# Kernel tuning notes

Hardware: AMD Instinct MI355X
Metric: run time of the kernel (lower is better)

Reference implementation:

```python
import jax, jax.numpy as jnp
import numpy as np
import math

D = 768; H = 12; DH = 64; LAT = 512; B = 2; L = 1024


def _rms(x, w, eps=1e-6):
    return w * x * jax.lax.rsqrt(jnp.mean(x * x, axis=-1, keepdims=True) + eps)


def _rope_tables(seq_len, dh):
    inv = 1.0 / (10000.0 ** (np.arange(0, dh, 2, dtype=np.float32) / dh))
    t = np.arange(seq_len, dtype=np.float32)
    f = np.outer(t, inv)
    emb = np.concatenate([f, f], axis=-1)
    return jnp.asarray(np.cos(emb))[None, :, None, :], jnp.asarray(np.sin(emb))[None, :, None, :]


def _rope(x, cos, sin):
    x1, x2 = jnp.split(x, 2, axis=-1)
    return x * cos + jnp.concatenate([-x2, x1], axis=-1) * sin


def setup_inputs():
    key = jax.random.key(0)
    ks = jax.random.split(key, 8)
    s = 0.02
    return {
        'x': jax.random.normal(ks[0], (B, L, D), jnp.float32),
        'w_ln': jnp.ones((D,), jnp.float32),
        'w_compress': jax.random.normal(ks[1], (D, LAT), jnp.float32) * s,
        'w_qkv': jax.random.normal(ks[2], (LAT, 3 * D), jnp.float32) * s,
        'w_reso': jax.random.normal(ks[3], (LAT, H * 4), jnp.float32) * s,
        'w_qn': jnp.ones((DH,), jnp.float32),
        'w_kn': jnp.ones((DH,), jnp.float32),
        'head_decay': jnp.linspace(-3.0, 1.0, H).astype(jnp.float32),
        'temperature': jnp.ones((1,), jnp.float32) * 0.5,
        'w_out_gate': jax.random.normal(ks[4], (LAT, D), jnp.float32) * s,
        'w_proj': jax.random.normal(ks[5], (D, D), jnp.float32) * s,
        'w_memnorm': jnp.ones((D,), jnp.float32),
    }


def reference(x, w_ln, w_compress, w_qkv, w_reso, w_qn, w_kn, head_decay, temperature, w_out_gate, w_proj, w_memnorm):
    cos, sin = _rope_tables(L, DH)
    xn = _rms(x, w_ln)
    latent = jax.nn.silu(xn @ w_compress)                        # (B,L,LAT)
    q, k, v = jnp.split(latent @ w_qkv, 3, axis=-1)
    q = _rope(_rms(q.reshape(B, L, H, DH), w_qn), cos, sin)
    k = _rope(_rms(k.reshape(B, L, H, DH), w_kn), cos, sin)
    v_f = v.reshape(B, L, H, DH)
    q_f = jax.nn.elu(q) + 1.0
    k_f = jax.nn.elu(k) + 1.0
    params = (latent @ w_reso).reshape(B, L, H, 4)
    sem_amp, sem_phase, ctx_amp, ctx_phase = [params[..., i] for i in range(4)]
    sem_phase = jax.nn.sigmoid(sem_phase) * math.pi
    ctx_phase = jax.nn.sigmoid(ctx_phase) * math.pi
    decay = jnp.clip(0.3 + 0.65 * jax.nn.sigmoid(head_decay), 1e-5, 0.999)   # (H,)
    gate = jnp.clip(jax.nn.sigmoid(jax.nn.sigmoid(sem_amp) * jax.nn.sigmoid(ctx_amp)
                                   * jnp.cos(sem_phase - ctx_phase) * temperature[0]) * 1.2 - 0.1,
                    0.05, 0.95)                                  # (B,L,H)
    one_m = (1.0 - decay)[None, None, :]                          # (1,1,H)
    kv_in = jnp.einsum('blhd,blhe->blhde', k_f, v_f) * gate[..., None, None] * one_m[..., None, None]
    z_in = k_f * one_m[..., None]
    # cumulative log-decay -> df, same as torch cumsum of constant per-step log_decay
    cum_log = jnp.arange(1, L + 1, dtype=jnp.float32)[:, None] * jnp.log(decay)[None, :]
    df = jnp.exp(cum_log)[None, :, :, None]                       # (1,L,H,1)
    kv_states = jnp.cumsum(kv_in / (df[..., None] + 1e-8), axis=1) * df[..., None]
    z_states = jnp.cumsum(z_in / (df + 1e-8), axis=1) * df
    out_num = jnp.einsum('blhd,blhde->blhe', q_f, kv_states)
    den = jnp.clip(jnp.sum(q_f * z_states, axis=-1, keepdims=True), 1e-5, None)
    out = (out_num / den).reshape(B, L, D)
    return (_rms(out, w_memnorm) @ w_proj) * jax.nn.silu(latent @ w_out_gate)
```

## Files before the change

### kernel.cpp

```cpp
#include <hip/hip_runtime.h>
#include <hip/hip_bf16.h>
#include <math.h>

#define D_MODEL 768
#define NHEAD   12
#define LATD    512
#define BATCH   2
#define SEQ     1024
#define NROWS   (BATCH*SEQ)
#define NCHUNK  (SEQ/64)
#define NBH     (BATCH*NHEAD)
#define NFUSE   3200
#define PQ      72

using short8 = __attribute__((ext_vector_type(8))) short;
using f32x4  = __attribute__((ext_vector_type(4))) float;

__device__ __forceinline__ float sigf(float x){ return 1.f/(1.f+expf(-x)); }
__device__ __forceinline__ float decay_of(float hd){
  float d = 0.3f + 0.65f*sigf(hd);
  return fminf(fmaxf(d, 1e-5f), 0.999f);
}
__device__ __forceinline__ unsigned short f2b(float f){
  __hip_bfloat16 h = __float2bfloat16(f);
  return *reinterpret_cast<unsigned short*>(&h);
}
__device__ __forceinline__ float bf2f(unsigned short u){
  unsigned int x = ((unsigned int)u) << 16;
  return __uint_as_float(x);
}
__device__ __forceinline__ void async16(const unsigned short* g, unsigned short* l){
  __builtin_amdgcn_global_load_lds((const __attribute__((address_space(1))) void*)g,
                                   (__attribute__((address_space(3))) void*)l, 16, 0, 0);
}

__device__ __forceinline__ void rms_row(const float* __restrict__ xr,
    const float* __restrict__ w, unsigned short* __restrict__ yr,
    int tid, float* red)
{
  float v0 = xr[tid], v1 = xr[tid+256], v2 = xr[tid+512];
  float s = v0*v0 + v1*v1 + v2*v2;
  #pragma unroll
  for (int off=32; off; off>>=1) s += __shfl_xor(s, off, 64);
  if ((tid & 63) == 0) red[tid>>6] = s;
  __syncthreads();
  s = red[0]+red[1]+red[2]+red[3];
  float sc = rsqrtf(s*(1.f/(float)D_MODEL) + 1e-6f);
  yr[tid]     = f2b(v0*sc*w[tid]);
  yr[tid+256] = f2b(v1*sc*w[tid+256]);
  yr[tid+512] = f2b(v2*sc*w[tid+512]);
}

__global__ __launch_bounds__(256) void k_rmsnorm_bf(const float* __restrict__ x,
    const float* __restrict__ w, unsigned short* __restrict__ y)
{
  __shared__ float red[4];
  int row = blockIdx.x, tid = threadIdx.x;
  rms_row(x + (size_t)row*D_MODEL, w, y + (size_t)row*D_MODEL, tid, red);
}

__global__ __launch_bounds__(256) void k_prep(
    const float* __restrict__ x, const float* __restrict__ w_ln,
    unsigned short* __restrict__ xn,
    const float* __restrict__ wc, const float* __restrict__ wq,
    const float* __restrict__ wr, const float* __restrict__ wg,
    const float* __restrict__ wp,
    unsigned short* __restrict__ wtc, unsigned short* __restrict__ wtq,
    unsigned short* __restrict__ wtg, unsigned short* __restrict__ wtp)
{
  __shared__ unsigned short tile[64][65];
  __shared__ float red[4];
  int blk = blockIdx.x, t = threadIdx.x;
  if (blk >= 640){
    int row = blk - 640;
    rms_row(x + (size_t)row*D_MODEL, w_ln, xn + (size_t)row*D_MODEL, t, red);
    return;
  }
  const float* W; unsigned short* WT; int K, N, bx, by;
  if (blk < 96){ W=wc; WT=wtc; K=768; N=512; bx=blk&7; by=blk>>3; }
  else if (blk < 384){ int i=blk-96;  W=wq; WT=wtq; K=512; N=2304; bx=i%36; by=i/36; }
  else if (blk < 480){ int i=blk-384; W=wg; WT=wtg; K=512; N=768;  bx=i%12; by=i/12; }
  else if (blk < 624){ int i=blk-480; W=wp; WT=wtp; K=768; N=768;  bx=i%12; by=i/12; }
  else {
    int i = blk - 624;
    #pragma unroll
    for (int j=0;j<16;j++){
      int e = i*4096 + t + j*256;
      int n = 2304 + (e >> 9), k = e & 511;
      float v = (n < 2352) ? wr[(size_t)k*48 + (n-2304)] : 0.f;
      wtq[(size_t)n*512 + k] = f2b(v);
    }
    return;
  }
  int k0 = by*64, n0 = bx*64, cr = t >> 6, cc = t & 63;
  #pragma unroll
  for (int i=0;i<16;i++){
    int r = cr + i*4;
    tile[r][cc] = f2b(W[(size_t)(k0+r)*N + n0 + cc]);
  }
  __syncthreads();
  #pragma unroll
  for (int i=0;i<16;i++){
    int nn = cr + i*4;
    WT[(size_t)(n0+nn)*K + k0 + cc] = tile[cc][nn];
  }
}

__global__ __launch_bounds__(256) void k_gemm64(const unsigned short* __restrict__ A,
    const unsigned short* __restrict__ BT, float* __restrict__ Cf,
    unsigned short* __restrict__ Cb, const unsigned short* __restrict__ auxb,
    int M, int N, int K, int act, int NX)
{
  __shared__ unsigned short As[64*64];
  __shared__ unsigned short Bs[64*64];
  int tid = threadIdx.x;
  int w = tid >> 6, lane = tid & 63;
  int m16 = lane & 15, quad = lane >> 4;
  int bid = blockIdx.x, cpx = gridDim.x >> 3;
  int swz = (bid & 7)*cpx + (bid >> 3);
  int bx = swz % NX, by = swz / NX;
  int bm = by*64, bn = bx*64;

  f32x4 acc[4];
  #pragma unroll
  for (int nt=0;nt<4;nt++) acc[nt] = (f32x4){0.f,0.f,0.f,0.f};

  for (int kk = 0; kk < K; kk += 64){
    #pragma unroll
    for (int i=0;i<2;i++){
      int g = (w*2 + i)*64 + lane;
      int m = g >> 3, c = (g & 7) ^ (m & 7);
      async16(A  + (size_t)(bm+m)*K + kk + c*8, As + (w*2+i)*512);
      async16(BT + (size_t)(bn+m)*K + kk + c*8, Bs + (w*2+i)*512);
    }
    __syncthreads();
    #pragma unroll
    for (int s=0;s<2;s++){
      int row = w*16 + m16;
      short8 af = *(const short8*)(As + (row*8 + ((s*4 + quad) ^ (row & 7)))*8);
      #pragma unroll
      for (int nt=0;nt<4;nt++){
        int n = nt*16 + m16;
        short8 bf = *(const short8*)(Bs + (n*8 + ((s*4 + quad) ^ (n & 7)))*8);
        acc[nt] = __builtin_amdgcn_mfma_f32_16x16x32_bf16(af, bf, acc[nt], 0, 0, 0);
      }
    }
    __syncthreads();
  }
  #pragma unroll
  for (int r=0;r<4;r++){
    int row = bm + w*16 + quad*4 + r;
    #pragma unroll
    for (int nt=0;nt<4;nt++){
      int col = bn + nt*16 + m16;
      float v = acc[nt][r];
      if (act == 1) v = v/(1.f + __expf(-v));
      else if (act == 2) v *= bf2f(auxb[(size_t)row*N + col]);
      if (Cf) Cf[(size_t)row*N + col] = v;
      if (Cb) Cb[(size_t)row*N + col] = f2b(v);
    }
  }
}

__global__ __launch_bounds__(256) void k_gemm_fused(const unsigned short* __restrict__ A,
    const unsigned short* __restrict__ BT, const float* __restrict__ w_qn,
    const float* __restrict__ w_kn, const float* __restrict__ hdec,
    const float* __restrict__ temp, unsigned short* __restrict__ qf,
    unsigned short* __restrict__ kf, unsigned short* __restrict__ vf,
    float* __restrict__ cKV, float* __restrict__ cG,
    unsigned short* __restrict__ gateb)
{
  __shared__ __align__(16) unsigned short SM[2*128*64];
  unsigned short* As = SM;
  unsigned short* Bs = SM + 128*64;
  const int K = LATD;
  int tid = threadIdx.x;
  int w = tid >> 6, lane = tid & 63;
  int wm = (w >> 1)*64, wn = (w & 1)*64;
  int m16 = lane & 15, quad = lane >> 4;
  int bid = blockIdx.x;
  int swz = (bid & 7)*50 + (bid >> 3);
  int bx = swz >> 4, by = swz & 15;
  int bm = by*128, bn = bx*128;

  f32x4 acc[4][4];
  #pragma unroll
  for (int i=0;i<4;i++)
    #pragma unroll
    for (int j=0;j<4;j++) acc[i][j] = (f32x4){0.f,0.f,0.f,0.f};

  for (int kk = 0; kk < K; kk += 64){
    #pragma unroll
    for (int i=0;i<4;i++){
      int g = (w*4 + i)*64 + lane;
      int m = g >> 3, c = (g & 7) ^ (m & 7);
      async16(A  + (size_t)(bm+m)*K + kk + c*8, As + (w*4+i)*512);
      async16(BT + (size_t)(bn+m)*K + kk + c*8, Bs + (w*4+i)*512);
    }
    __syncthreads();
    #pragma unroll
    for (int s=0;s<2;s++){
      short8 af[4], bf[4];
      #pragma unroll
      for (int mt=0;mt<4;mt++){
        int m = wm + mt*16 + m16;
        int idx = m*8 + ((s*4 + quad) ^ (m & 7));
        af[mt] = *(const short8*)(As + idx*8);
      }
      #pragma unroll
      for (int nt=0;nt<4;nt++){
        int n = wn + nt*16 + m16;
        int idx = n*8 + ((s*4 + quad) ^ (n & 7));
        bf[nt] = *(const short8*)(Bs + idx*8);
      }
      #pragma unroll
      for (int mt=0;mt<4;mt++)
        #pragma unroll
        for (int nt=0;nt<4;nt++)
          acc[mt][nt] = __builtin_amdgcn_mfma_f32_16x16x32_bf16(af[mt], bf[nt], acc[mt][nt], 0, 0, 0);
    }
    __syncthreads();
  }

  int colbase = bn + wn;
  if (colbase < 2304){
    int sec = colbase >= 1536 ? 2 : (colbase >= 768 ? 1 : 0);
    int h = (colbase - sec*768) >> 6;
    if (sec == 2){
      #pragma unroll
      for (int mt=0;mt<4;mt++)
        #pragma unroll
        for (int r=0;r<4;r++){
          int row = bm + wm + mt*16 + quad*4 + r;
          int b = row >> 10, t = row & 1023;
          size_t ob = (((size_t)(b*NHEAD+h))*SEQ + t)*64;
          #pragma unroll
          for (int nt=0;nt<4;nt++)
            vf[ob + nt*16 + m16] = f2b(acc[mt][nt][r]);
        }
    } else {
      const float* wnp = sec ? w_kn : w_qn;
      unsigned short* of = sec ? kf : qf;
      float wv4[4];
      #pragma unroll
      for (int nt=0;nt<4;nt++) wv4[nt] = wnp[nt*16 + m16];
      float inv0 = exp2f(-(float)m16*(1.f/32.f)*13.28771237954945f);
      float inv1 = inv0 * 0.01f;
      #pragma unroll
      for (int mt=0;mt<4;mt++)
        #pragma unroll
        for (int r=0;r<4;r++){
          int row = bm + wm + mt*16 + quad*4 + r;
          int b = row >> 10, t = row & 1023;
          float s = 0.f;
          #pragma unroll
          for (int nt=0;nt<4;nt++) s += acc[mt][nt][r]*acc[mt][nt][r];
          s += __shfl_xor(s, 1, 64); s += __shfl_xor(s, 2, 64);
          s += __shfl_xor(s, 4, 64); s += __shfl_xor(s, 8, 64);
          float rs = rsqrtf(s*(1.f/64.f) + 1e-6f);
          float qv[4];
          #pragma unroll
          for (int nt=0;nt<4;nt++) qv[nt] = acc[mt][nt][r]*rs*wv4[nt];
          float s0,c0,s1,c1;
          __sincosf((float)t*inv0, &s0, &c0);
          __sincosf((float)t*inv1, &s1, &c1);
          size_t ob = (((size_t)(b*NHEAD+h))*SEQ + t)*64;
          #pragma unroll
          for (int nt=0;nt<4;nt++){
            float rot = (nt < 2) ? -qv[nt+2] : qv[nt-2];
            float cs = (nt & 1) ? c1 : c0, sn = (nt & 1) ? s1 : s0;
            float val = qv[nt]*cs + rot*sn;
            val = (val > 0.f) ? val + 1.f : __expf(val);
            of[ob + nt*16 + m16] = f2b(val);
          }
        }
    }
  } else if (colbase < 2432){
    float* pf = (float*)SM;
    if (colbase == 2304){
      #pragma unroll
      for (int mt=0;mt<4;mt++)
        #pragma unroll
        for (int r=0;r<4;r++){
          int rowl = wm + mt*16 + quad*4 + r;
          #pragma unroll
          for (int nt=0;nt<4;nt++){
            int p = nt*16 + m16;
            if (p < 48) pf[rowl*49 + p] = acc[mt][nt][r];
          }
        }
    }
    __syncthreads();
    float tv = temp[0];
    #pragma unroll
    for (int i=0;i<6;i++){
      int idx2 = tid + i*256;
      int rowl = idx2 / 12, h = idx2 - rowl*12;
      int row = bm + rowl, b = row >> 10, t = row & 1023;
      const float* pr = pf + rowl*49 + h*4;
      float sa = sigf(pr[0]);
      float sp = sigf(pr[1])*3.14159265358979323846f;
      float ca = sigf(pr[2]);
      float cp = sigf(pr[3])*3.14159265358979323846f;
      float z = sa*ca*cosf(sp - cp)*tv;
      float gate = fminf(fmaxf(sigf(z)*1.2f - 0.1f, 0.05f), 0.95f);
      float dd = decay_of(hdec[h]);
      float df = expf((float)(t+1)*logf(dd));
      float g = df/(df + 1e-8f);
      int ci = (b*NHEAD + h)*SEQ + t;
      cKV[ci] = g*gate*(1.f - dd);
      cG[ci]  = 1.f/gate;
    }
  } else {
    #pragma unroll
    for (int mt=0;mt<4;mt++)
      #pragma unroll
      for (int r=0;r<4;r++){
        int row = bm + wm + mt*16 + quad*4 + r;
        #pragma unroll
        for (int nt=0;nt<4;nt++){
          int gc = colbase + nt*16 + m16 - 2432;
          float v = acc[mt][nt][r];
          v = v/(1.f + __expf(-v));
          gateb[(size_t)row*D_MODEL + gc] = f2b(v);
        }
      }
  }
}

__global__ __launch_bounds__(256) void k_intra(const unsigned short* __restrict__ qf,
    const unsigned short* __restrict__ kf, const unsigned short* __restrict__ vf,
    const float* __restrict__ cKVb, const float* __restrict__ cGb,
    const float* __restrict__ hdec, float* __restrict__ numb,
    float* __restrict__ denb, float* __restrict__ Pb, float* __restrict__ zPb)
{
  __shared__ __align__(16) unsigned short Qb[64*PQ];
  __shared__ __align__(16) unsigned short Kb[64*PQ];
  __shared__ __align__(16) unsigned short KtS[64*PQ];
  __shared__ __align__(16) unsigned short Wb[64*PQ];
  __shared__ __align__(16) unsigned short Vt[80*PQ];
  __shared__ float cn[64], cps[64];
  int bid = blockIdx.x;
  int chunk = bid & 15, bh = bid >> 4, h = bh % NHEAD;
  int tid = threadIdx.x, w = tid >> 6, lane = tid & 63;
  int m16 = lane & 15, quad = lane >> 4;
  size_t base = ((size_t)bh*SEQ + chunk*64)*64;
  float d = decay_of(hdec[h]);
  float l2d = log2f(d);

  if (tid < 64){
    float c = cKVb[bh*SEQ + chunk*64 + tid];
    float pw = exp2f((float)(63 - tid)*l2d);
    cn[tid] = c;
    cps[tid] = c*pw;
    Vt[64*PQ + tid] = f2b(cGb[bh*SEQ + chunk*64 + tid]);
  }
  for (int i = tid; i < 15*PQ; i += 256) Vt[65*PQ + i] = 0;
  __syncthreads();

  #pragma unroll
  for (int i=0;i<2;i++){
    int g = tid + i*256;
    int r = g >> 3, c8 = (g & 7)*8;
    *(short8*)(Qb + r*PQ + c8) = *(const short8*)(qf + base + r*64 + c8);
    *(short8*)(Kb + r*PQ + c8) = *(const short8*)(kf + base + r*64 + c8);
  }
  {
    int s = tid & 63;
    float cpss = cps[s];
    #pragma unroll
    for (int i=0;i<2;i++){
      int c8 = ((tid >> 6) + i*4)*8;
      short8 vv = *(const short8*)(vf + base + s*64 + c8);
      short8 kk = *(const short8*)(kf + base + s*64 + c8);
      #pragma unroll
      for (int j=0;j<8;j++){
        Vt[(c8+j)*PQ + s] = ((unsigned short*)&vv)[j];
        KtS[(c8+j)*PQ + s] = f2b(bf2f(((unsigned short*)&kk)[j])*cpss);
      }
    }
  }
  __syncthreads();

  int trow = w*16 + quad*4;
  for (int stile=0; stile<4; stile++){
    if (stile > w){
      #pragma unroll
      for (int r=0;r<4;r++) Wb[(trow+r)*PQ + stile*16 + m16] = 0;
      continue;
    }
    f32x4 acc = (f32x4){0.f,0.f,0.f,0.f};
    #pragma unroll
    for (int ks=0;ks<2;ks++){
      short8 a = *(const short8*)(Qb + (w*16 + m16)*PQ + ks*32 + quad*8);
      short8 b = *(const short8*)(Kb + (stile*16 + m16)*PQ + ks*32 + quad*8);
      acc = __builtin_amdgcn_mfma_f32_16x16x32_bf16(a, b, acc, 0, 0, 0);
    }
    int s = stile*16 + m16;
    float cns = cn[s];
    #pragma unroll
    for (int r=0;r<4;r++){
      int t = trow + r;
      float wv = 0.f;
      if (s <= t) wv = acc[r]*exp2f((float)(t-s)*l2d)*cns;
      Wb[t*PQ + s] = f2b(wv);
    }
  }
  __syncthreads();

  {
    f32x4 acc[5];
    #pragma unroll
    for (int et=0;et<5;et++) acc[et] = (f32x4){0.f,0.f,0.f,0.f};
    #pragma unroll
    for (int et=0;et<5;et++)
      #pragma unroll
      for (int ks=0;ks<2;ks++){
        short8 a = *(const short8*)(Wb + (w*16 + m16)*PQ + ks*32 + quad*8);
        short8 b = *(const short8*)(Vt + (et*16 + m16)*PQ + ks*32 + quad*8);
        acc[et] = __builtin_amdgcn_mfma_f32_16x16x32_bf16(a, b, acc[et], 0, 0, 0);
      }
    #pragma unroll
    for (int et=0;et<4;et++)
      #pragma unroll
      for (int r=0;r<4;r++)
        numb[base + (size_t)(trow+r)*64 + et*16 + m16] = acc[et][r];
    if (m16 == 0){
      #pragma unroll
      for (int r=0;r<4;r++)
        denb[bh*SEQ + chunk*64 + trow + r] = acc[4][r];
    }
  }
  {
    #pragma unroll
    for (int j=0;j<5;j++){
      int tIdx = w + 4*j;
      int et = tIdx >> 2, dt = tIdx & 3;
      f32x4 acc = (f32x4){0.f,0.f,0.f,0.f};
      #pragma unroll
      for (int ks=0;ks<2;ks++){
        short8 a = *(const short8*)(Vt  + (et*16 + m16)*PQ + ks*32 + quad*8);
        short8 b = *(const short8*)(KtS + (dt*16 + m16)*PQ + ks*32 + quad*8);
        acc = __builtin_amdgcn_mfma_f32_16x16x32_bf16(a, b, acc, 0, 0, 0);
      }
      if (et < 4){
        #pragma unroll
        for (int r=0;r<4;r++)
          Pb[(size_t)bid*4096 + (et*16 + quad*4 + r)*64 + dt*16 + m16] = acc[r];
      } else {
        if (quad == 0) zPb[bid*64 + dt*16 + m16] = acc[0];
      }
    }
  }
}

__global__ __launch_bounds__(256) void k_cross(const unsigned short* __restrict__ qf,
    const float* __restrict__ Pb, const float* __restrict__ zPb,
    const float* __restrict__ numb, const float* __restrict__ denb,
    const float* __restrict__ hdec, float* __restrict__ attn)
{
  __shared__ __align__(16) unsigned short Qb[64*PQ];
  __shared__ __align__(16) unsigned short Sp[80*PQ];
  __shared__ float den_sm[64];
  int bid = blockIdx.x;
  int swz = (bid & 7)*48 + (bid >> 3);
  int chunk = swz & 15, bh = swz >> 4;
  int h = bh % NHEAD, b = bh / NHEAD;
  int tid = threadIdx.x, w = tid >> 6, lane = tid & 63;
  int m16 = lane & 15, quad = lane >> 4;
  size_t base = ((size_t)bh*SEQ + chunk*64)*64;
  float d = decay_of(hdec[h]);
  float l2d = log2f(d);
  float d64l2 = 64.f*l2d;

  #pragma unroll
  for (int i=0;i<2;i++){
    int g = tid + i*256;
    int r = g >> 3, c8 = (g & 7)*8;
    *(short8*)(Qb + r*PQ + c8) = *(const short8*)(qf + base + r*64 + c8);
  }

  {
    int r = tid >> 3, c8 = (tid & 7)*8;
    float a0[8], a1[8];
    #pragma unroll
    for (int j=0;j<8;j++){ a0[j]=0.f; a1[j]=0.f; }
    for (int c=0;c<chunk;c++){
      float wgt = exp2f((float)(chunk-1-c)*d64l2);
      const float* ps = Pb + ((size_t)(bh*NCHUNK + c))*4096;
      float4 p0 = *(const float4*)(ps + r*64 + c8);
      float4 p1 = *(const float4*)(ps + r*64 + c8 + 4);
      float4 p2 = *(const float4*)(ps + (r+32)*64 + c8);
      float4 p3 = *(const float4*)(ps + (r+32)*64 + c8 + 4);
      a0[0]+=wgt*p0.x; a0[1]+=wgt*p0.y; a0[2]+=wgt*p0.z; a0[3]+=wgt*p0.w;
      a0[4]+=wgt*p1.x; a0[5]+=wgt*p1.y; a0[6]+=wgt*p1.z; a0[7]+=wgt*p1.w;
      a1[0]+=wgt*p2.x; a1[1]+=wgt*p2.y; a1[2]+=wgt*p2.z; a1[3]+=wgt*p2.w;
      a1[4]+=wgt*p3.x; a1[5]+=wgt*p3.y; a1[6]+=wgt*p3.z; a1[7]+=wgt*p3.w;
    }
    #pragma unroll
    for (int j=0;j<8;j++){
      Sp[r*PQ + c8 + j]      = f2b(a0[j]);
      Sp[(r+32)*PQ + c8 + j] = f2b(a1[j]);
    }
  }
  if (tid < 64){
    float z = 0.f;
    for (int c=0;c<chunk;c++)
      z += exp2f((float)(chunk-1-c)*d64l2) * zPb[(bh*NCHUNK + c)*64 + tid];
    Sp[64*PQ + tid] = f2b(z);
  }
  for (int i = tid; i < 15*PQ; i += 256) Sp[65*PQ + i] = 0;
  __syncthreads();

  f32x4 acc[5];
  #pragma unroll
  for (int et=0;et<5;et++) acc[et] = (f32x4){0.f,0.f,0.f,0.f};
  #pragma unroll
  for (int et=0;et<5;et++)
    #pragma unroll
    for (int ks=0;ks<2;ks++){
      short8 a = *(const short8*)(Qb + (w*16 + m16)*PQ + ks*32 + quad*8);
      short8 bb = *(const short8*)(Sp + (et*16 + m16)*PQ + ks*32 + quad*8);
      acc[et] = __builtin_amdgcn_mfma_f32_16x16x32_bf16(a, bb, acc[et], 0, 0, 0);
    }
  int trow = w*16 + quad*4;
  if (m16 == 0){
    #pragma unroll
    for (int r=0;r<4;r++){
      int tl = trow + r;
      float pw = exp2f((float)(tl+1)*l2d);
      float den = fmaxf(denb[bh*SEQ + chunk*64 + tl] + pw*acc[4][r], 1e-5f);
      den_sm[tl] = 1.f/den;
    }
  }
  __syncthreads();
  #pragma unroll
  for (int r=0;r<4;r++){
    int tl = trow + r;
    float pw = exp2f((float)(tl+1)*l2d);
    float invden = den_sm[tl];
    int tg = chunk*64 + tl;
    #pragma unroll
    for (int et=0;et<4;et++){
      int e = et*16 + m16;
      float nm = numb[base + (size_t)tl*64 + e] + pw*acc[et][r];
      attn[((size_t)(b*SEQ + tg))*D_MODEL + h*64 + e] = nm*invden;
    }
  }
}

extern "C" void kernel_launch(void* const* d_in, const int* in_sizes, int n_in,
                              void* d_out, int out_size, void* d_ws, size_t ws_size,
                              hipStream_t stream)
{
  (void)in_sizes; (void)n_in; (void)out_size; (void)ws_size;
  const float* x       = (const float*)d_in[0];
  const float* w_ln    = (const float*)d_in[1];
  const float* w_comp  = (const float*)d_in[2];
  const float* w_qkv   = (const float*)d_in[3];
  const float* w_reso  = (const float*)d_in[4];
  const float* w_qn    = (const float*)d_in[5];
  const float* w_kn    = (const float*)d_in[6];
  const float* hdec    = (const float*)d_in[7];
  const float* temp    = (const float*)d_in[8];
  const float* w_ogate = (const float*)d_in[9];
  const float* w_proj  = (const float*)d_in[10];
  const float* w_mn    = (const float*)d_in[11];
  float* ws = (float*)d_ws;
  float* out = (float*)d_out;

  const size_t o_cKV    = 0;
  const size_t o_cG     = o_cKV    + (size_t)NBH*SEQ;
  const size_t o_den    = o_cG     + (size_t)NBH*SEQ;
  const size_t o_P      = o_den    + (size_t)NBH*SEQ;
  const size_t o_zP     = o_P      + (size_t)NBH*NCHUNK*4096;
  const size_t o_attn   = o_zP     + (size_t)NBH*NCHUNK*64;
  const size_t o_numb   = o_attn   + (size_t)NROWS*D_MODEL;
  const size_t o_end    = o_numb   + (size_t)NBH*SEQ*64;

  unsigned short* bws = (unsigned short*)(ws + o_end);
  const size_t u_xn     = 0;
  const size_t u_latent = u_xn     + (size_t)NROWS*D_MODEL;
  const size_t u_memn   = u_latent + (size_t)NROWS*LATD;
  const size_t u_q      = u_memn   + (size_t)NROWS*D_MODEL;
  const size_t u_k      = u_q      + (size_t)NBH*SEQ*64;
  const size_t u_v      = u_k      + (size_t)NBH*SEQ*64;
  const size_t u_gate   = u_v      + (size_t)NBH*SEQ*64;
  const size_t u_wtc    = u_gate   + (size_t)NROWS*D_MODEL;
  const size_t u_wtq    = u_wtc    + (size_t)LATD*D_MODEL;
  const size_t u_wtg    = u_wtq    + (size_t)2432*LATD;
  const size_t u_wtp    = u_wtg    + (size_t)D_MODEL*LATD;

  k_prep<<<2688, 256, 0, stream>>>(x, w_ln, bws + u_xn,
      w_comp, w_qkv, w_reso, w_ogate, w_proj,
      bws + u_wtc, bws + u_wtq, bws + u_wtg, bws + u_wtp);
  k_gemm64<<<256, 256, 0, stream>>>(bws + u_xn, bws + u_wtc,
      nullptr, bws + u_latent, nullptr, NROWS, LATD, D_MODEL, 1, LATD/64);
  k_gemm_fused<<<400, 256, 0, stream>>>(bws + u_latent, bws + u_wtq,
      w_qn, w_kn, hdec, temp, bws + u_q, bws + u_k, bws + u_v,
      ws + o_cKV, ws + o_cG, bws + u_gate);
  k_intra<<<NBH*NCHUNK, 256, 0, stream>>>(bws + u_q, bws + u_k, bws + u_v,
      ws + o_cKV, ws + o_cG, hdec, ws + o_numb, ws + o_den, ws + o_P, ws + o_zP);
  k_cross<<<NBH*NCHUNK, 256, 0, stream>>>(bws + u_q, ws + o_P, ws + o_zP,
      ws + o_numb, ws + o_den, hdec, ws + o_attn);
  k_rmsnorm_bf<<<NROWS, 256, 0, stream>>>(ws + o_attn, w_mn, bws + u_memn);
  k_gemm64<<<384, 256, 0, stream>>>(bws + u_memn, bws + u_wtp,
      out, nullptr, bws + u_gate, NROWS, D_MODEL, D_MODEL, 2, D_MODEL/64);
}
```

Baseline: 157.4 us.

## Double-buffer LDS tiles in both bf16 GEMM kernels to overlap loads with MFMA

Both the 64x64 GEMM and the fused 128x128 QKV GEMM now keep two shared-memory stages. The next K-tile's async global-to-LDS copy is issued before the MFMA work on the current tile, and one barrier per iteration replaces two. The aim is to hide global load latency behind matrix math and cut synchronisation. In exchange, shared memory per block doubles (to 64 KB in the fused kernel), which can lower occupancy. Overlap may also be limited if the barrier waits on all outstanding vector memory operations.

```diff
diff --git a/kernel.cpp b/kernel.cpp
--- a/kernel.cpp
+++ b/kernel.cpp
@@ -111,8 +111,8 @@
     unsigned short* __restrict__ Cb, const unsigned short* __restrict__ auxb,
     int M, int N, int K, int act, int NX)
 {
-  __shared__ unsigned short As[64*64];
-  __shared__ unsigned short Bs[64*64];
+  __shared__ unsigned short As[2*64*64];
+  __shared__ unsigned short Bs[2*64*64];
   int tid = threadIdx.x;
   int w = tid >> 6, lane = tid & 63;
   int m16 = lane & 15, quad = lane >> 4;
@@ -125,27 +125,41 @@
   #pragma unroll
   for (int nt=0;nt<4;nt++) acc[nt] = (f32x4){0.f,0.f,0.f,0.f};
 
-  for (int kk = 0; kk < K; kk += 64){
-    #pragma unroll
-    for (int i=0;i<2;i++){
-      int g = (w*2 + i)*64 + lane;
-      int m = g >> 3, c = (g & 7) ^ (m & 7);
-      async16(A  + (size_t)(bm+m)*K + kk + c*8, As + (w*2+i)*512);
-      async16(BT + (size_t)(bn+m)*K + kk + c*8, Bs + (w*2+i)*512);
-    }
-    __syncthreads();
+  int nk = K >> 6;
+  #pragma unroll
+  for (int i=0;i<2;i++){
+    int g = (w*2 + i)*64 + lane;
+    int m = g >> 3, c = (g & 7) ^ (m & 7);
+    async16(A  + (size_t)(bm+m)*K + c*8, As + (w*2+i)*512);
+    async16(BT + (size_t)(bn+m)*K + c*8, Bs + (w*2+i)*512);
+  }
+  __syncthreads();
+  int cur = 0;
+  for (int t = 0; t < nk; ++t){
+    if (t+1 < nk){
+      int kk = (t+1) << 6;
+      int nb = cur ^ 1;
+      #pragma unroll
+      for (int i=0;i<2;i++){
+        int g = (w*2 + i)*64 + lane;
+        int m = g >> 3, c = (g & 7) ^ (m & 7);
+        async16(A  + (size_t)(bm+m)*K + kk + c*8, As + nb*4096 + (w*2+i)*512);
+        async16(BT + (size_t)(bn+m)*K + kk + c*8, Bs + nb*4096 + (w*2+i)*512);
+      }
+    }
     #pragma unroll
     for (int s=0;s<2;s++){
       int row = w*16 + m16;
-      short8 af = *(const short8*)(As + (row*8 + ((s*4 + quad) ^ (row & 7)))*8);
+      short8 af = *(const short8*)(As + cur*4096 + (row*8 + ((s*4 + quad) ^ (row & 7)))*8);
       #pragma unroll
       for (int nt=0;nt<4;nt++){
         int n = nt*16 + m16;
-        short8 bf = *(const short8*)(Bs + (n*8 + ((s*4 + quad) ^ (n & 7)))*8);
+        short8 bf = *(const short8*)(Bs + cur*4096 + (n*8 + ((s*4 + quad) ^ (n & 7)))*8);
         acc[nt] = __builtin_amdgcn_mfma_f32_16x16x32_bf16(af, bf, acc[nt], 0, 0, 0);
       }
     }
     __syncthreads();
+    cur ^= 1;
   }
   #pragma unroll
   for (int r=0;r<4;r++){
@@ -170,9 +184,9 @@
     float* __restrict__ cKV, float* __restrict__ cG,
     unsigned short* __restrict__ gateb)
 {
-  __shared__ __align__(16) unsigned short SM[2*128*64];
+  __shared__ __align__(16) unsigned short SM[4*128*64];
   unsigned short* As = SM;
-  unsigned short* Bs = SM + 128*64;
+  unsigned short* Bs = SM + 2*128*64;
   const int K = LATD;
   int tid = threadIdx.x;
   int w = tid >> 6, lane = tid & 63;
@@ -189,15 +203,28 @@
     #pragma unroll
     for (int j=0;j<4;j++) acc[i][j] = (f32x4){0.f,0.f,0.f,0.f};
 
-  for (int kk = 0; kk < K; kk += 64){
-    #pragma unroll
-    for (int i=0;i<4;i++){
-      int g = (w*4 + i)*64 + lane;
-      int m = g >> 3, c = (g & 7) ^ (m & 7);
-      async16(A  + (size_t)(bm+m)*K + kk + c*8, As + (w*4+i)*512);
-      async16(BT + (size_t)(bn+m)*K + kk + c*8, Bs + (w*4+i)*512);
-    }
-    __syncthreads();
+  const int nk = K >> 6;
+  #pragma unroll
+  for (int i=0;i<4;i++){
+    int g = (w*4 + i)*64 + lane;
+    int m = g >> 3, c = (g & 7) ^ (m & 7);
+    async16(A  + (size_t)(bm+m)*K + c*8, As + (w*4+i)*512);
+    async16(BT + (size_t)(bn+m)*K + c*8, Bs + (w*4+i)*512);
+  }
+  __syncthreads();
+  int cur = 0;
+  for (int t = 0; t < nk; ++t){
+    if (t+1 < nk){
+      int kk = (t+1) << 6;
+      int nb = cur ^ 1;
+      #pragma unroll
+      for (int i=0;i<4;i++){
+        int g = (w*4 + i)*64 + lane;
+        int m = g >> 3, c = (g & 7) ^ (m & 7);
+        async16(A  + (size_t)(bm+m)*K + kk + c*8, As + nb*8192 + (w*4+i)*512);
+        async16(BT + (size_t)(bn+m)*K + kk + c*8, Bs + nb*8192 + (w*4+i)*512);
+      }
+    }
     #pragma unroll
     for (int s=0;s<2;s++){
       short8 af[4], bf[4];
@@ -205,13 +232,13 @@
       for (int mt=0;mt<4;mt++){
         int m = wm + mt*16 + m16;
         int idx = m*8 + ((s*4 + quad) ^ (m & 7));
-        af[mt] = *(const short8*)(As + idx*8);
+        af[mt] = *(const short8*)(As + cur*8192 + idx*8);
       }
       #pragma unroll
       for (int nt=0;nt<4;nt++){
         int n = wn + nt*16 + m16;
         int idx = n*8 + ((s*4 + quad) ^ (n & 7));
-        bf[nt] = *(const short8*)(Bs + idx*8);
+        bf[nt] = *(const short8*)(Bs + cur*8192 + idx*8);
       }
       #pragma unroll
       for (int mt=0;mt<4;mt++)
@@ -220,6 +247,7 @@
           acc[mt][nt] = __builtin_amdgcn_mfma_f32_16x16x32_bf16(af[mt], bf[nt], acc[mt][nt], 0, 0, 0);
     }
     __syncthreads();
+    cur ^= 1;
   }
 
   int colbase = bn + wn;
```

After: 150.3 us. -4.5%, faster.
